# Optimization experiments

Measured on AMD Instinct MI355X. Metric: run time of the kernel, lower is better.

Reference implementation:

```python
import jax, jax.numpy as jnp
import numpy as np

B, T, C = 2, 2048, 1024
NH = 16
HD = C // NH


def setup_inputs() -> dict:
    key = jax.random.key(0)
    k1, k2, k3 = jax.random.split(key, 3)
    x = jax.random.normal(k1, (B, T, C), dtype=jnp.float32)
    w_qkv = jax.random.normal(k2, (C, 3 * C), dtype=jnp.float32) * (C ** -0.5)
    w_proj = jax.random.normal(k3, (C, C), dtype=jnp.float32) * (C ** -0.5)
    return {"x": x, "w_qkv": w_qkv, "w_proj": w_proj}


def reference(x, w_qkv, w_proj):
    Bv, Tv, Cv = x.shape
    qkv = x @ w_qkv  # [B, T, 3C]
    q, k, v = jnp.split(qkv, 3, axis=-1)
    # [B, T, C] -> [B, NH, T, HD]
    q = q.reshape(Bv, Tv, NH, HD).transpose(0, 2, 1, 3)
    k = k.reshape(Bv, Tv, NH, HD).transpose(0, 2, 1, 3)
    v = v.reshape(Bv, Tv, NH, HD).transpose(0, 2, 1, 3)
    att = jnp.einsum("bhqd,bhkd->bhqk", q, k) * (HD ** -0.5)
    causal = jnp.tril(jnp.ones((Tv, Tv), dtype=bool))  # [T, T]
    att = jnp.where(causal[None, None, :, :], att, -jnp.inf)
    att = jax.nn.softmax(att, axis=-1)
    # dropout p=0.0 (eval) -> identity
    y = jnp.einsum("bhqk,bhkd->bhqd", att, v)  # [B, NH, T, HD]
    y = y.transpose(0, 2, 1, 3).reshape(Bv, Tv, Cv)
    return y @ w_proj
```

## Files before the change

kernel.cpp:

```cpp
#include <hip/hip_runtime.h>
#include <hip/hip_bf16.h>

#define B_ 2
#define T_ 2048
#define C_ 1024
#define NH_ 16
#define HD_ 64

using bf16 = __hip_bfloat16;
typedef __attribute__((ext_vector_type(8))) short bf16x8;
typedef __attribute__((ext_vector_type(4))) float f32x4;

__device__ __forceinline__ float bf2f(unsigned short u) {
    union { unsigned int i; float f; } v;
    v.i = ((unsigned int)u) << 16;
    return v.f;
}
__device__ __forceinline__ unsigned short f2bf(float f) {
    union { float f; unsigned int u; } v;
    v.f = f;
    unsigned int r = v.u + 0x7fffu + ((v.u >> 16) & 1u);
    return (unsigned short)(r >> 16);
}
__device__ __forceinline__ unsigned int cvt_pk_bf16(float lo, float hi) {
    unsigned int r;
    asm("v_cvt_pk_bf16_f32 %0, %1, %2" : "=v"(r) : "v"(lo), "v"(hi));
    return r;
}
__device__ __forceinline__ void gld_lds16(const void* g, void* l) {
    __builtin_amdgcn_global_load_lds(
        (__attribute__((address_space(1))) void*)g,
        (__attribute__((address_space(3))) void*)l, 16, 0, 0);
}

__global__ __launch_bounds__(256) void prep(
    const float* __restrict__ X, const float* __restrict__ Wq,
    const float* __restrict__ Wp,
    unsigned short* __restrict__ Xb, unsigned short* __restrict__ Wqt,
    unsigned short* __restrict__ Wpt) {
    __shared__ short S[64][72];
    const int b = blockIdx.x;
    const int t = threadIdx.x;
    if (b < 2048) {
        int i = (b * 256 + t) * 8;
        float4 f0 = *reinterpret_cast<const float4*>(&X[i]);
        float4 f1 = *reinterpret_cast<const float4*>(&X[i + 4]);
        union { unsigned short s[8]; uint4 v; } o;
        o.s[0] = f2bf(f0.x); o.s[1] = f2bf(f0.y); o.s[2] = f2bf(f0.z); o.s[3] = f2bf(f0.w);
        o.s[4] = f2bf(f1.x); o.s[5] = f2bf(f1.y); o.s[6] = f2bf(f1.z); o.s[7] = f2bf(f1.w);
        *reinterpret_cast<uint4*>(&Xb[i]) = o.v;
        return;
    }
    const int lr = t >> 2, lc = (t & 3) * 16;
    const float* src;
    unsigned short* dstbase;
    int NN, KK, n0, k0;
    if (b < 2816) {
        const int idx = b - 2048;
        n0 = (idx % 48) * 64; k0 = (idx / 48) * 64;
        NN = 3 * C_; KK = C_;
        src = &Wq[(size_t)(k0 + lr) * NN + n0 + lc];
        dstbase = Wqt;
    } else {
        const int idx = b - 2816;
        n0 = (idx & 15) * 64; k0 = (idx >> 4) * 64;
        NN = C_; KK = C_;
        src = &Wp[(size_t)(k0 + lr) * NN + n0 + lc];
        dstbase = Wpt;
    }
    #pragma unroll
    for (int j4 = 0; j4 < 4; ++j4) {
        float4 f = *reinterpret_cast<const float4*>(src + j4 * 4);
        S[lc + j4 * 4 + 0][lr] = (short)f2bf(f.x);
        S[lc + j4 * 4 + 1][lr] = (short)f2bf(f.y);
        S[lc + j4 * 4 + 2][lr] = (short)f2bf(f.z);
        S[lc + j4 * 4 + 3][lr] = (short)f2bf(f.w);
    }
    __syncthreads();
    union { unsigned short s[16]; uint4 v[2]; } o;
    #pragma unroll
    for (int j = 0; j < 16; ++j) o.s[j] = (unsigned short)S[lr][lc + j];
    unsigned short* dst = &dstbase[(size_t)(n0 + lr) * KK + k0 + lc];
    *reinterpret_cast<uint4*>(dst)     = o.v[0];
    *reinterpret_cast<uint4*>(dst + 8) = o.v[1];
}

__global__ __launch_bounds__(256) void post(
    const unsigned short* __restrict__ V, unsigned short* __restrict__ Vt) {
    __shared__ short S[64][72];
    const int b = blockIdx.x;
    const int t = threadIdx.x;
    const int lr = t >> 2, lc = (t & 3) * 16;
    const int bh = b >> 5, t0 = (b & 31) * 64;
    const unsigned short* src = V + ((size_t)bh * T_ + t0 + lr) * HD_ + lc;
    union { uint4 v[2]; unsigned short s[16]; } u;
    u.v[0] = *reinterpret_cast<const uint4*>(src);
    u.v[1] = *reinterpret_cast<const uint4*>(src + 8);
    #pragma unroll
    for (int j = 0; j < 16; ++j) S[lc + j][lr] = (short)u.s[j];
    __syncthreads();
    union { unsigned short s[16]; uint4 v[2]; } o;
    #pragma unroll
    for (int j = 0; j < 16; ++j) o.s[j] = (unsigned short)S[lr][lc + j];
    unsigned short* dst = Vt + ((size_t)bh * HD_ + lr) * T_ + t0 + lc;
    *reinterpret_cast<uint4*>(dst)     = o.v[0];
    *reinterpret_cast<uint4*>(dst + 8) = o.v[1];
}

__global__ __launch_bounds__(256) void qkv_gemm_mfma(
    const unsigned short* __restrict__ A, const unsigned short* __restrict__ Bt,
    unsigned short* __restrict__ Qb, unsigned short* __restrict__ Kb,
    unsigned short* __restrict__ Vb) {
    __shared__ short As[2][128 * 32];
    __shared__ short Bs[2][128 * 32];
    const int t = threadIdx.x;
    const int wid = t >> 6, lane = t & 63;
    const int wm = wid >> 1, wn = wid & 1;
    const int c = lane & 15, g = lane >> 4;
    const int dd = blockIdx.x;
    const int w  = (dd & 7) * 96 + (dd >> 3);
    const int m0 = (w / 24) * 128, n0 = (w % 24) * 128;
    const int K = C_;
    const int srow = t >> 2, skk = (t & 3) * 8;

    f32x4 acc[4][4];
    #pragma unroll
    for (int i = 0; i < 4; ++i)
        #pragma unroll
        for (int j = 0; j < 4; ++j) acc[i][j] = (f32x4){0.f, 0.f, 0.f, 0.f};

    gld_lds16(&A[(size_t)(m0 + srow) * K + skk],       As[0] + t * 8);
    gld_lds16(&A[(size_t)(m0 + 64 + srow) * K + skk],  As[0] + 2048 + t * 8);
    gld_lds16(&Bt[(size_t)(n0 + srow) * K + skk],      Bs[0] + t * 8);
    gld_lds16(&Bt[(size_t)(n0 + 64 + srow) * K + skk], Bs[0] + 2048 + t * 8);

    #pragma unroll 1
    for (int kt = 0; kt < 32; ++kt) {
        const int cur = kt & 1;
        __syncthreads();
        if (kt < 31) {
            const int k0 = (kt + 1) * 32;
            gld_lds16(&A[(size_t)(m0 + srow) * K + k0 + skk],       As[cur ^ 1] + t * 8);
            gld_lds16(&A[(size_t)(m0 + 64 + srow) * K + k0 + skk],  As[cur ^ 1] + 2048 + t * 8);
            gld_lds16(&Bt[(size_t)(n0 + srow) * K + k0 + skk],      Bs[cur ^ 1] + t * 8);
            gld_lds16(&Bt[(size_t)(n0 + 64 + srow) * K + k0 + skk], Bs[cur ^ 1] + 2048 + t * 8);
        }
        bf16x8 af[4], bfv[4];
        #pragma unroll
        for (int mi = 0; mi < 4; ++mi)
            af[mi] = *reinterpret_cast<const bf16x8*>(&As[cur][(wm * 64 + mi * 16 + c) * 32 + g * 8]);
        #pragma unroll
        for (int ni = 0; ni < 4; ++ni)
            bfv[ni] = *reinterpret_cast<const bf16x8*>(&Bs[cur][(wn * 64 + ni * 16 + c) * 32 + g * 8]);
        #pragma unroll
        for (int mi = 0; mi < 4; ++mi)
            #pragma unroll
            for (int ni = 0; ni < 4; ++ni)
                acc[mi][ni] = __builtin_amdgcn_mfma_f32_16x16x32_bf16(af[mi], bfv[ni], acc[mi][ni], 0, 0, 0);
    }

    const int nbase = n0 + wn * 64;
    const int which = nbase >> 10;
    const int h     = (nbase >> 6) & (NH_ - 1);
    const float scale = (which == 0) ? 0.125f * 1.44269504f : 1.0f;
    unsigned short* dst = (which == 0) ? Qb : ((which == 1) ? Kb : Vb);
    #pragma unroll
    for (int mi = 0; mi < 4; ++mi)
        #pragma unroll
        for (int r = 0; r < 4; ++r) {
            const int m = m0 + wm * 64 + mi * 16 + 4 * g + r;
            const int bb = m >> 11, tq = m & (T_ - 1);
            unsigned short* p = dst + ((size_t)((bb << 4) | h) * T_ + tq) * HD_;
            #pragma unroll
            for (int ni = 0; ni < 4; ++ni)
                p[ni * 16 + c] = f2bf(acc[mi][ni][r] * scale);
        }
}

__global__ __launch_bounds__(256) void proj_gemm_mfma(
    const unsigned short* __restrict__ A, const unsigned short* __restrict__ Bt,
    float* __restrict__ Out) {
    __shared__ short As[2][64 * 32];
    __shared__ short Bs[2][128 * 32];
    const int t = threadIdx.x;
    const int wid = t >> 6, lane = t & 63;
    const int wm = wid >> 1, wn = wid & 1;
    const int c = lane & 15, g = lane >> 4;
    const int dd = blockIdx.x;
    const int w  = (dd & 7) * 64 + (dd >> 3);
    const int m0 = (w >> 3) * 64, n0 = (w & 7) * 128;
    const int K = C_;
    const int srow = t >> 2, skk = (t & 3) * 8;

    f32x4 acc[2][4];
    #pragma unroll
    for (int i = 0; i < 2; ++i)
        #pragma unroll
        for (int j = 0; j < 4; ++j) acc[i][j] = (f32x4){0.f, 0.f, 0.f, 0.f};

    gld_lds16(&A[(size_t)(m0 + srow) * K + skk],       As[0] + t * 8);
    gld_lds16(&Bt[(size_t)(n0 + srow) * K + skk],      Bs[0] + t * 8);
    gld_lds16(&Bt[(size_t)(n0 + 64 + srow) * K + skk], Bs[0] + 2048 + t * 8);

    #pragma unroll 1
    for (int kt = 0; kt < 32; ++kt) {
        const int cur = kt & 1;
        __syncthreads();
        if (kt < 31) {
            const int k0 = (kt + 1) * 32;
            gld_lds16(&A[(size_t)(m0 + srow) * K + k0 + skk],       As[cur ^ 1] + t * 8);
            gld_lds16(&Bt[(size_t)(n0 + srow) * K + k0 + skk],      Bs[cur ^ 1] + t * 8);
            gld_lds16(&Bt[(size_t)(n0 + 64 + srow) * K + k0 + skk], Bs[cur ^ 1] + 2048 + t * 8);
        }
        bf16x8 af[2], bfv[4];
        #pragma unroll
        for (int mi = 0; mi < 2; ++mi)
            af[mi] = *reinterpret_cast<const bf16x8*>(&As[cur][(wm * 32 + mi * 16 + c) * 32 + g * 8]);
        #pragma unroll
        for (int ni = 0; ni < 4; ++ni)
            bfv[ni] = *reinterpret_cast<const bf16x8*>(&Bs[cur][(wn * 64 + ni * 16 + c) * 32 + g * 8]);
        #pragma unroll
        for (int mi = 0; mi < 2; ++mi)
            #pragma unroll
            for (int ni = 0; ni < 4; ++ni)
                acc[mi][ni] = __builtin_amdgcn_mfma_f32_16x16x32_bf16(af[mi], bfv[ni], acc[mi][ni], 0, 0, 0);
    }

    #pragma unroll
    for (int mi = 0; mi < 2; ++mi)
        #pragma unroll
        for (int r = 0; r < 4; ++r) {
            const int m = m0 + wm * 32 + mi * 16 + 4 * g + r;
            float* p = Out + (size_t)m * C_ + n0 + wn * 64;
            #pragma unroll
            for (int ni = 0; ni < 4; ++ni)
                p[ni * 16 + c] = acc[mi][ni][r];
        }
}

__global__ __launch_bounds__(512) void attn_mfma(
    const unsigned short* __restrict__ Qb, const unsigned short* __restrict__ Kb,
    const unsigned short* __restrict__ Vt_g, unsigned short* __restrict__ Yu) {
    __shared__ short Ks[2][64][72];
    __shared__ short Vt[2][64][72];

    const int t    = threadIdx.x;
    const int wid  = t >> 6;
    const int lane = t & 63;
    const int c    = lane & 15;
    const int g    = lane >> 4;

    const int d   = blockIdx.x;
    const int xcd = d & 7;
    const int tt  = d >> 3;
    const int up  = tt & 15;
    const int k2  = tt >> 4;
    const int bh  = (k2 << 3) | xcd;
    const int u   = (k2 & 2) ? (15 - up) : up;
    const int qtB = 2 * u + 1;
    const int myqt = (wid < 4) ? (2 * u) : qtB;

    const int bb = bh >> 4, h = bh & (NH_ - 1);
    const int qw0 = (wid & 3) * 16;
    const int q0  = myqt * 64;

    const unsigned short* Qh  = Qb   + (size_t)bh * T_ * HD_;
    const unsigned short* Kh  = Kb   + (size_t)bh * T_ * HD_;
    const unsigned short* VTh = Vt_g + (size_t)bh * HD_ * T_;

    const int srow = t >> 3, scol = (t & 7) * 8;
    const int jA = scol, jB = scol + 4;
    const int slotA = 32 * (jA >> 5) + 8 * ((jA >> 2) & 3) + 4 * ((jA >> 4) & 1);
    const int slotB = 32 * (jB >> 5) + 8 * ((jB >> 2) & 3) + 4 * ((jB >> 4) & 1);

    bf16x8 qf0, qf1;
    {
        const unsigned short* qs = Qh + (size_t)(q0 + qw0 + c) * HD_ + g * 8;
        qf0 = *reinterpret_cast<const bf16x8*>(qs);
        qf1 = *reinterpret_cast<const bf16x8*>(qs + 32);
    }

    float l_run = 0.f;
    f32x4 yacc[4];
    #pragma unroll
    for (int nt = 0; nt < 4; ++nt) yacc[nt] = (f32x4){0.f, 0.f, 0.f, 0.f};

    uint4 kv, vv;
    {
        kv = *reinterpret_cast<const uint4*>(&Kh[(size_t)srow * HD_ + scol]);
        vv = *reinterpret_cast<const uint4*>(&VTh[(size_t)srow * T_ + scol]);
    }

    #pragma unroll 1
    for (int kt = 0; kt <= qtB; ++kt) {
        const int cur = kt & 1;
        *reinterpret_cast<uint4*>(&Ks[cur][srow][scol]) = kv;
        *reinterpret_cast<uint2*>(&Vt[cur][srow][slotA]) = make_uint2(vv.x, vv.y);
        *reinterpret_cast<uint2*>(&Vt[cur][srow][slotB]) = make_uint2(vv.z, vv.w);
        __syncthreads();

        if (kt < qtB) {
            const int j1 = (kt + 1) * 64;
            kv = *reinterpret_cast<const uint4*>(&Kh[(size_t)(j1 + srow) * HD_ + scol]);
            vv = *reinterpret_cast<const uint4*>(&VTh[(size_t)srow * T_ + j1 + scol]);
        }

        if (kt <= myqt) {
            f32x4 sacc[4];
            #pragma unroll
            for (int nt = 0; nt < 4; ++nt) sacc[nt] = (f32x4){0.f, 0.f, 0.f, 0.f};
            __builtin_amdgcn_s_setprio(1);
            #pragma unroll
            for (int kk = 0; kk < 2; ++kk) {
                const bf16x8 qf = kk ? qf1 : qf0;
                #pragma unroll
                for (int nt = 0; nt < 4; ++nt) {
                    bf16x8 kf = *reinterpret_cast<const bf16x8*>(&Ks[cur][nt * 16 + c][kk * 32 + g * 8]);
                    sacc[nt] = __builtin_amdgcn_mfma_f32_16x16x32_bf16(kf, qf, sacc[nt], 0, 0, 0);
                }
            }
            __builtin_amdgcn_s_setprio(0);

            const bool diag = (kt == myqt);
            float p[4][4];
            float lsum = 0.f;
            #pragma unroll
            for (int nt = 0; nt < 4; ++nt)
                #pragma unroll
                for (int r = 0; r < 4; ++r) {
                    float s = sacc[nt][r];
                    if (diag && (nt * 16 + 4 * g + r > qw0 + c)) s = -1e30f;
                    float pv = exp2f(s);
                    p[nt][r] = pv;
                    lsum += pv;
                }
            l_run += lsum;

            unsigned int pk[8];
            #pragma unroll
            for (int nt = 0; nt < 4; ++nt) {
                pk[2 * nt]     = cvt_pk_bf16(p[nt][0], p[nt][1]);
                pk[2 * nt + 1] = cvt_pk_bf16(p[nt][2], p[nt][3]);
            }

            __builtin_amdgcn_s_setprio(1);
            #pragma unroll
            for (int kk = 0; kk < 2; ++kk) {
                union { unsigned int w[4]; bf16x8 v; } pa;
                pa.w[0] = pk[4 * kk + 0]; pa.w[1] = pk[4 * kk + 1];
                pa.w[2] = pk[4 * kk + 2]; pa.w[3] = pk[4 * kk + 3];
                #pragma unroll
                for (int nt = 0; nt < 4; ++nt) {
                    bf16x8 vb = *reinterpret_cast<const bf16x8*>(&Vt[cur][nt * 16 + c][kk * 32 + g * 8]);
                    yacc[nt] = __builtin_amdgcn_mfma_f32_16x16x32_bf16(pa.v, vb, yacc[nt], 0, 0, 0);
                }
            }
            __builtin_amdgcn_s_setprio(0);
        }
    }

    float lf = l_run;
    lf += __shfl_xor(lf, 16, 64);
    lf += __shfl_xor(lf, 32, 64);
    const float inv = 1.0f / lf;
    const int ii = __float_as_int(inv);
    float invr[4];
    #pragma unroll
    for (int r = 0; r < 4; ++r)
        invr[r] = __int_as_float(__builtin_amdgcn_ds_bpermute((4 * g + r) * 4, ii));
    #pragma unroll
    for (int r = 0; r < 4; ++r) {
        const size_t row = (size_t)(bb * T_ + q0 + qw0 + 4 * g + r);
        #pragma unroll
        for (int nt = 0; nt < 4; ++nt) {
            const int col = h * HD_ + 16 * nt + c;
            Yu[row * C_ + col] = f2bf(yacc[nt][r] * invr[r]);
        }
    }
}

extern "C" void kernel_launch(void* const* d_in, const int* in_sizes, int n_in,
                              void* d_out, int out_size, void* d_ws, size_t ws_size,
                              hipStream_t stream) {
    const float* x      = (const float*)d_in[0];
    const float* w_qkv  = (const float*)d_in[1];
    const float* w_proj = (const float*)d_in[2];
    float* out = (float*)d_out;

    const size_t HELEMS = (size_t)B_ * NH_ * T_ * HD_;
    unsigned short* Qb   = (unsigned short*)d_ws;
    unsigned short* Kb   = Qb + HELEMS;
    unsigned short* Vraw = Kb + HELEMS;
    unsigned short* Yb   = Vraw;
    unsigned short* Xb   = Vraw + HELEMS;
    unsigned short* Vt   = Xb;
    unsigned short* Wqt  = Xb + HELEMS;
    unsigned short* Wpt  = Wqt + (size_t)3 * C_ * C_;

    prep<<<3072, 256, 0, stream>>>(x, w_qkv, w_proj, Xb, Wqt, Wpt);
    qkv_gemm_mfma<<<768, 256, 0, stream>>>(Xb, Wqt, Qb, Kb, Vraw);
    post<<<1024, 256, 0, stream>>>(Vraw, Vt);
    attn_mfma<<<512, 512, 0, stream>>>(Qb, Kb, Vt, Yb);
    proj_gemm_mfma<<<512, 256, 0, stream>>>(Yb, Wpt, out);
}
```

Measured before the change: 107.9 us.

## Fuse fp32-to-bf16 conversion of X into the QKV GEMM operand load

Removes the separate X conversion pass from the prep kernel and instead has the QKV GEMM load fp32 X directly through registers, converting to bf16 with packed cvt instructions before writing into LDS. This avoids writing and rereading a bf16 copy of X, and prep launches fewer blocks. In exchange, the A operand no longer uses direct global-to-LDS loads: fp32 data is read twice per M-tile across the 24 N-tiles, so A reads carry double the bytes. The register prefetch also adds VGPR pressure and places conversion work on the GEMM's critical path.

```diff
diff --git a/kernel.cpp b/kernel.cpp
--- a/kernel.cpp
+++ b/kernel.cpp
@@ -34,35 +34,22 @@
 }
 
 __global__ __launch_bounds__(256) void prep(
-    const float* __restrict__ X, const float* __restrict__ Wq,
-    const float* __restrict__ Wp,
-    unsigned short* __restrict__ Xb, unsigned short* __restrict__ Wqt,
-    unsigned short* __restrict__ Wpt) {
+    const float* __restrict__ Wq, const float* __restrict__ Wp,
+    unsigned short* __restrict__ Wqt, unsigned short* __restrict__ Wpt) {
     __shared__ short S[64][72];
     const int b = blockIdx.x;
     const int t = threadIdx.x;
-    if (b < 2048) {
-        int i = (b * 256 + t) * 8;
-        float4 f0 = *reinterpret_cast<const float4*>(&X[i]);
-        float4 f1 = *reinterpret_cast<const float4*>(&X[i + 4]);
-        union { unsigned short s[8]; uint4 v; } o;
-        o.s[0] = f2bf(f0.x); o.s[1] = f2bf(f0.y); o.s[2] = f2bf(f0.z); o.s[3] = f2bf(f0.w);
-        o.s[4] = f2bf(f1.x); o.s[5] = f2bf(f1.y); o.s[6] = f2bf(f1.z); o.s[7] = f2bf(f1.w);
-        *reinterpret_cast<uint4*>(&Xb[i]) = o.v;
-        return;
-    }
     const int lr = t >> 2, lc = (t & 3) * 16;
     const float* src;
     unsigned short* dstbase;
     int NN, KK, n0, k0;
-    if (b < 2816) {
-        const int idx = b - 2048;
-        n0 = (idx % 48) * 64; k0 = (idx / 48) * 64;
+    if (b < 768) {
+        n0 = (b % 48) * 64; k0 = (b / 48) * 64;
         NN = 3 * C_; KK = C_;
         src = &Wq[(size_t)(k0 + lr) * NN + n0 + lc];
         dstbase = Wqt;
     } else {
-        const int idx = b - 2816;
+        const int idx = b - 768;
         n0 = (idx & 15) * 64; k0 = (idx >> 4) * 64;
         NN = C_; KK = C_;
         src = &Wp[(size_t)(k0 + lr) * NN + n0 + lc];
@@ -108,7 +95,7 @@
 }
 
 __global__ __launch_bounds__(256) void qkv_gemm_mfma(
-    const unsigned short* __restrict__ A, const unsigned short* __restrict__ Bt,
+    const float* __restrict__ X, const unsigned short* __restrict__ Bt,
     unsigned short* __restrict__ Qb, unsigned short* __restrict__ Kb,
     unsigned short* __restrict__ Vb) {
     __shared__ short As[2][128 * 32];
@@ -129,21 +116,39 @@
         #pragma unroll
         for (int j = 0; j < 4; ++j) acc[i][j] = (f32x4){0.f, 0.f, 0.f, 0.f};
 
-    gld_lds16(&A[(size_t)(m0 + srow) * K + skk],       As[0] + t * 8);
-    gld_lds16(&A[(size_t)(m0 + 64 + srow) * K + skk],  As[0] + 2048 + t * 8);
+    const float* Xa = &X[(size_t)(m0 + srow) * K + skk];
+    const float* Xb2 = &X[(size_t)(m0 + 64 + srow) * K + skk];
+
+    float4 a0, a1, b0, b1;
+    a0 = *reinterpret_cast<const float4*>(Xa);
+    a1 = *reinterpret_cast<const float4*>(Xa + 4);
+    b0 = *reinterpret_cast<const float4*>(Xb2);
+    b1 = *reinterpret_cast<const float4*>(Xb2 + 4);
     gld_lds16(&Bt[(size_t)(n0 + srow) * K + skk],      Bs[0] + t * 8);
     gld_lds16(&Bt[(size_t)(n0 + 64 + srow) * K + skk], Bs[0] + 2048 + t * 8);
 
     #pragma unroll 1
     for (int kt = 0; kt < 32; ++kt) {
         const int cur = kt & 1;
+        {
+            union { unsigned int w[4]; uint4 v; } p0, p1;
+            p0.w[0] = cvt_pk_bf16(a0.x, a0.y); p0.w[1] = cvt_pk_bf16(a0.z, a0.w);
+            p0.w[2] = cvt_pk_bf16(a1.x, a1.y); p0.w[3] = cvt_pk_bf16(a1.z, a1.w);
+            p1.w[0] = cvt_pk_bf16(b0.x, b0.y); p1.w[1] = cvt_pk_bf16(b0.z, b0.w);
+            p1.w[2] = cvt_pk_bf16(b1.x, b1.y); p1.w[3] = cvt_pk_bf16(b1.z, b1.w);
+            *reinterpret_cast<uint4*>(&As[cur][t * 8])        = p0.v;
+            *reinterpret_cast<uint4*>(&As[cur][2048 + t * 8]) = p1.v;
+        }
         __syncthreads();
+
         if (kt < 31) {
             const int k0 = (kt + 1) * 32;
-            gld_lds16(&A[(size_t)(m0 + srow) * K + k0 + skk],       As[cur ^ 1] + t * 8);
-            gld_lds16(&A[(size_t)(m0 + 64 + srow) * K + k0 + skk],  As[cur ^ 1] + 2048 + t * 8);
             gld_lds16(&Bt[(size_t)(n0 + srow) * K + k0 + skk],      Bs[cur ^ 1] + t * 8);
             gld_lds16(&Bt[(size_t)(n0 + 64 + srow) * K + k0 + skk], Bs[cur ^ 1] + 2048 + t * 8);
+            a0 = *reinterpret_cast<const float4*>(Xa + k0);
+            a1 = *reinterpret_cast<const float4*>(Xa + k0 + 4);
+            b0 = *reinterpret_cast<const float4*>(Xb2 + k0);
+            b1 = *reinterpret_cast<const float4*>(Xb2 + k0 + 4);
         }
         bf16x8 af[4], bfv[4];
         #pragma unroll
@@ -392,13 +397,12 @@
     unsigned short* Kb   = Qb + HELEMS;
     unsigned short* Vraw = Kb + HELEMS;
     unsigned short* Yb   = Vraw;
-    unsigned short* Xb   = Vraw + HELEMS;
-    unsigned short* Vt   = Xb;
-    unsigned short* Wqt  = Xb + HELEMS;
+    unsigned short* Vt   = Vraw + HELEMS;
+    unsigned short* Wqt  = Vt + HELEMS;
     unsigned short* Wpt  = Wqt + (size_t)3 * C_ * C_;
 
-    prep<<<3072, 256, 0, stream>>>(x, w_qkv, w_proj, Xb, Wqt, Wpt);
-    qkv_gemm_mfma<<<768, 256, 0, stream>>>(Xb, Wqt, Qb, Kb, Vraw);
+    prep<<<1024, 256, 0, stream>>>(w_qkv, w_proj, Wqt, Wpt);
+    qkv_gemm_mfma<<<768, 256, 0, stream>>>(x, Wqt, Qb, Kb, Vraw);
     post<<<1024, 256, 0, stream>>>(Vraw, Vt);
     attn_mfma<<<512, 512, 0, stream>>>(Qb, Kb, Vt, Yb);
     proj_gemm_mfma<<<512, 256, 0, stream>>>(Yb, Wpt, out);
```

Measured after the change: 108.8 us. No clear change (+0.8%).
